# Performance work log

Hardware: AMD Instinct MI355X
Metric: run time of the kernel (lower is better)

## Reference

```python
import jax, jax.numpy as jnp
import numpy as np

B, S, N = 1, 128, 256
C_IN, C_H, C_OUT = 256, 32, 128
EPS = 1e-5


def setup_inputs() -> dict:
    key = jax.random.key(0)
    k_m, k_wa, k_wb, k_wo = jax.random.split(key, 4)
    m = jax.random.normal(k_m, (B, S, N, C_IN), dtype=jnp.float32)
    mask = jnp.ones((B, S, N), dtype=jnp.float32)
    gamma = jnp.ones((C_IN,), dtype=jnp.float32)
    beta = jnp.zeros((C_IN,), dtype=jnp.float32)
    # nn.Linear weights are (out, in)
    Wa = jax.random.normal(k_wa, (C_H, C_IN), dtype=jnp.float32) / np.sqrt(C_IN).astype(np.float32)
    Wb = jax.random.normal(k_wb, (C_H, C_IN), dtype=jnp.float32) / np.sqrt(C_IN).astype(np.float32)
    # proj_o is final_init (zeros) in the source; use small random weights so the
    # baseline output is non-trivial for correctness checking.
    Wo = jax.random.normal(k_wo, (C_OUT, C_H * C_H), dtype=jnp.float32) / np.sqrt(C_H * C_H).astype(np.float32)
    bo = jnp.zeros((C_OUT,), dtype=jnp.float32)
    return {"m": m, "mask": mask, "gamma": gamma, "beta": beta,
            "Wa": Wa, "Wb": Wb, "Wo": Wo, "bo": bo}


def reference(m, mask, gamma, beta, Wa, Wb, Wo, bo):
    # LayerNorm over c_in
    mu = jnp.mean(m, axis=-1, keepdims=True)
    var = jnp.mean((m - mu) ** 2, axis=-1, keepdims=True)
    mn = (m - mu) * jax.lax.rsqrt(var + EPS) * gamma + beta  # (B,S,N,c_in)

    mk = mask[..., None]  # (B,S,N,1)
    a = jnp.einsum('bsni,hi->bsnh', mn, Wa) * mk  # (B,S,N,c_h)
    b = jnp.einsum('bsni,hi->bsnh', mn, Wb) * mk  # (B,S,N,c_h)

    # pairwise mask count over S, clamped to >= 1
    num_mask = jnp.clip(jnp.einsum('bsi,bsj->bij', mask, mask), 1.0, None)  # (B,N,N)

    # outer-product mean over the sequence dim
    z = jnp.einsum('bsic,bsjd->bijcd', a, b)  # (B,N,N,c_h,c_h)
    z = z.reshape(z.shape[0], z.shape[1], z.shape[2], C_H * C_H)
    z = z / num_mask[..., None]

    return jnp.einsum('bijk,ok->bijo', z, Wo) + bo  # (B,N,N,c_out)
```

## Files before the change

### kernel.cpp

```cpp
#include <hip/hip_runtime.h>
#include <hip/hip_bf16.h>

#define S_DIM 128
#define N_DIM 256
#define CIN   256
#define CH    32
#define COUT  128

typedef __attribute__((ext_vector_type(8))) short bf16x8;
typedef __attribute__((ext_vector_type(4))) float f32x4;
typedef __attribute__((ext_vector_type(16))) float f32x16;

__device__ __forceinline__ unsigned short f2bf(float f) {
  union { float f; unsigned int u; } v; v.f = f;
  unsigned int u = v.u;
  return (unsigned short)((u + 0x7FFFu + ((u >> 16) & 1u)) >> 16);
}

__device__ __forceinline__ unsigned int pk2(float x, float y) {
  float2 f2; f2.x = x; f2.y = y;
  __hip_bfloat162 h = __float22bfloat162_rn(f2);
  union { __hip_bfloat162 h; unsigned int u; } c; c.h = h;
  return c.u;
}

__global__ __launch_bounds__(256) void lnp_prep_kernel(
    const float* __restrict__ m, const float* __restrict__ mask,
    const float* __restrict__ gamma, const float* __restrict__ beta,
    const float* __restrict__ Wa, const float* __restrict__ Wb,
    const float* __restrict__ Wo,
    float* __restrict__ rnm, unsigned short* __restrict__ wo3,
    unsigned short* __restrict__ a_t, unsigned short* __restrict__ b_t) {
  const int b = blockIdx.x, t = threadIdx.x;
  if (b < 1024) {
    __shared__ __align__(16) unsigned short mn[32][264];
    __shared__ __align__(16) unsigned short wabs[64 * 256];
    const int i = b & 255, s0 = (b >> 8) * 32;
    const int w = t >> 6, l = t & 63, lq = l >> 4, lr = l & 15;

    #pragma unroll
    for (int it = 0; it < 8; it++) {
      const int gi = it * 256 + t;
      const int r = gi >> 5, g = gi & 31;
      const float* src = (r < 32) ? (Wa + r * 256 + g * 8)
                                  : (Wb + (r - 32) * 256 + g * 8);
      const int gp = (g & 16) | ((g ^ (r & 15)) & 15);
      unsigned short* dst = &wabs[r * 256 + gp * 8];
      const float4 v0 = *(const float4*)(src);
      const float4 v1 = *(const float4*)(src + 4);
      dst[0] = f2bf(v0.x); dst[1] = f2bf(v0.y); dst[2] = f2bf(v0.z); dst[3] = f2bf(v0.w);
      dst[4] = f2bf(v1.x); dst[5] = f2bf(v1.y); dst[6] = f2bf(v1.z); dst[7] = f2bf(v1.w);
    }

    const float4 g4 = *(const float4*)(gamma + l * 4);
    const float4 b4 = *(const float4*)(beta + l * 4);

    for (int rr = 0; rr < 8; rr++) {
      const int r = w * 8 + rr;
      const int s = s0 + r;
      const float4 v = *(const float4*)(m + ((size_t)(s * N_DIM + i)) * CIN + l * 4);
      float sum = v.x + v.y + v.z + v.w;
      float sq  = v.x * v.x + v.y * v.y + v.z * v.z + v.w * v.w;
      #pragma unroll
      for (int off = 32; off > 0; off >>= 1) {
        sum += __shfl_down(sum, off);
        sq  += __shfl_down(sq, off);
      }
      sum = __shfl(sum, 0); sq = __shfl(sq, 0);
      const float mu = sum * (1.0f / CIN);
      const float var = fmaxf(sq * (1.0f / CIN) - mu * mu, 0.0f);
      const float rs = rsqrtf(var + 1e-5f);
      const float mk = mask[s * N_DIM + i];
      ushort4 p;
      p.x = f2bf(((v.x - mu) * rs * g4.x + b4.x) * mk);
      p.y = f2bf(((v.y - mu) * rs * g4.y + b4.y) * mk);
      p.z = f2bf(((v.z - mu) * rs * g4.z + b4.z) * mk);
      p.w = f2bf(((v.w - mu) * rs * g4.w + b4.w) * mk);
      *(ushort4*)(&mn[r][l * 4]) = p;
    }
    __syncthreads();

    const int wm = w & 1;
    const int n2 = w >> 1;
    f32x4 acc0 = {0.f, 0.f, 0.f, 0.f}, acc1 = {0.f, 0.f, 0.f, 0.f};
    #pragma unroll
    for (int ks = 0; ks < 8; ks++) {
      const int k0 = ks * 32 + lq * 8;
      const int g = ks * 4 + lq;
      const int gp = (g & 16) | ((g ^ lr) & 15);
      const bf16x8 af = *(const bf16x8*)(&mn[wm * 16 + lr][k0]);
      const bf16x8 bf0 = *(const bf16x8*)(&wabs[(n2 * 32 + lr) * 256 + gp * 8]);
      const bf16x8 bf1 = *(const bf16x8*)(&wabs[(n2 * 32 + 16 + lr) * 256 + gp * 8]);
      acc0 = __builtin_amdgcn_mfma_f32_16x16x32_bf16(af, bf0, acc0, 0, 0, 0);
      acc1 = __builtin_amdgcn_mfma_f32_16x16x32_bf16(af, bf1, acc1, 0, 0, 0);
    }

    unsigned short* dst = (n2 == 0) ? a_t : b_t;
    const int scol = s0 + wm * 16 + lq * 4;
    ushort4 q0, q1;
    q0.x = f2bf(acc0[0]); q0.y = f2bf(acc0[1]); q0.z = f2bf(acc0[2]); q0.w = f2bf(acc0[3]);
    q1.x = f2bf(acc1[0]); q1.y = f2bf(acc1[1]); q1.z = f2bf(acc1[2]); q1.w = f2bf(acc1[3]);
    *(ushort4*)(dst + ((size_t)(i * CH + lr)) * S_DIM + scol) = q0;
    *(ushort4*)(dst + ((size_t)(i * CH + 16 + lr)) * S_DIM + scol) = q1;
  } else if (b < 1152) {
    const int r = b - 1024;
    #pragma unroll
    for (int q = 0; q < 4; q++) {
      const int f = r * 1024 + q * 256 + t;
      const int e = f & 7, l = (f >> 3) & 63;
      const int step = (f >> 9) & 63, og = f >> 15;
      const int kp = step * 16 + (l >> 5) * 8 + e;
      const int c = kp & 31, d = kp >> 5;
      const int o = og * 32 + (l & 31);
      wo3[f] = f2bf(Wo[o * 1024 + c * 32 + d]);
    }
  } else {
    const int i = b - 1152;
    float acc = 0.f;
    #pragma unroll 8
    for (int s = 0; s < S_DIM; s++)
      acc += mask[s * N_DIM + i] * mask[s * N_DIM + t];
    acc = fmaxf(acc, 1.0f);
    rnm[i * N_DIM + t] = 1.0f / acc;
  }
}

__global__ __launch_bounds__(1024, 4) void fused_kernel(
    const unsigned short* __restrict__ a_t, const unsigned short* __restrict__ b_t,
    const unsigned short* __restrict__ wo3, const float* __restrict__ rnm,
    const float* __restrict__ bo, float* __restrict__ out) {
  extern __shared__ __align__(16) unsigned short smem[];
  unsigned short* sA = smem;
  unsigned short* sB = smem + 32768;
  unsigned short* sZ = smem;
  float* fpart = (float*)smem;

  const int t = threadIdx.x, w = t >> 6, l = t & 63;
  const int lq = l >> 4, lr = l & 15;
  const int bx = blockIdx.x, by = blockIdx.y;

  const unsigned short* srcA = a_t + (size_t)bx * 32768;
  const unsigned short* srcB = b_t + (size_t)by * 32768;
  #pragma unroll
  for (int it = 0; it < 4; it++) {
    const int idx = it * 1024 + t;
    const int r = idx >> 4, g = idx & 15;
    const int dst = r * 128 + ((g ^ (r & 15)) * 8);
    *(bf16x8*)(&sA[dst]) = *(const bf16x8*)(srcA + idx * 8);
    *(bf16x8*)(&sB[dst]) = *(const bf16x8*)(srcB + idx * 8);
  }
  __syncthreads();

  const int wy = (w >> 2) * 64, wx = (w & 3) * 64;
  f32x4 acc[4][4];
  #pragma unroll
  for (int a = 0; a < 4; a++)
    #pragma unroll
    for (int c = 0; c < 4; c++) acc[a][c] = (f32x4){0.f, 0.f, 0.f, 0.f};

  #pragma unroll
  for (int ks = 0; ks < 4; ks++) {
    const int g0 = ks * 4 + lq;
    bf16x8 afr[4], bfr[4];
    #pragma unroll
    for (int a = 0; a < 4; a++) {
      const int ra = wy + a * 16 + lr;
      afr[a] = *(const bf16x8*)(&sA[ra * 128 + ((g0 ^ (ra & 15)) * 8)]);
      const int rb = wx + a * 16 + lr;
      bfr[a] = *(const bf16x8*)(&sB[rb * 128 + ((g0 ^ (rb & 15)) * 8)]);
    }
    #pragma unroll
    for (int a = 0; a < 4; a++)
      #pragma unroll
      for (int c = 0; c < 4; c++)
        acc[a][c] = __builtin_amdgcn_mfma_f32_16x16x32_bf16(afr[a], bfr[c], acc[a][c], 0, 0, 0);
  }
  __syncthreads();

  #pragma unroll
  for (int a = 0; a < 4; a++) {
    #pragma unroll
    for (int c = 0; c < 4; c++) {
      const int zrb = wy + a * 16 + lq * 4;
      const int zc  = wx + c * 16 + lr;
      const int pr = (zrb >> 5) * 8 + (zc >> 5);
      const int off = (zc & 31) * 32 + (zrb & 31);
      const int g = off >> 3;
      const int gp = (g & ~7) | ((g ^ (g >> 3) ^ pr) & 7);
      uint2 q;
      q.x = pk2(acc[a][c][0], acc[a][c][1]);
      q.y = pk2(acc[a][c][2], acc[a][c][3]);
      *(uint2*)(&sZ[pr * 1024 + gp * 8 + (off & 7)]) = q;
    }
  }
  __syncthreads();

  const int og = w & 3, kq = w >> 2;
  const int pA = l & 31, pB = 32 + pA;
  const unsigned short* wop =
      wo3 + ((size_t)(og * 64 + kq * 16) * 64 + l) * 8;
  f32x16 accA, accB;
  #pragma unroll
  for (int r = 0; r < 16; r++) { accA[r] = 0.f; accB[r] = 0.f; }

  #pragma unroll 8
  for (int j = 0; j < 16; j++) {
    const int s = kq * 16 + j;
    const int g = s * 2 + (l >> 5);
    const int gA = (g & ~7) | ((g ^ (g >> 3) ^ pA) & 7);
    const int gB = (g & ~7) | ((g ^ (g >> 3) ^ pB) & 7);
    const bf16x8 zfA = *(const bf16x8*)(&sZ[pA * 1024 + gA * 8]);
    const bf16x8 zfB = *(const bf16x8*)(&sZ[pB * 1024 + gB * 8]);
    const bf16x8 wf = *(const bf16x8*)(wop + (size_t)j * 512);
    accA = __builtin_amdgcn_mfma_f32_32x32x16_bf16(zfA, wf, accA, 0, 0, 0);
    accB = __builtin_amdgcn_mfma_f32_32x32x16_bf16(zfB, wf, accB, 0, 0, 0);
  }
  __syncthreads();

  const int oc = og * 32 + (l & 31);
  #pragma unroll
  for (int r = 0; r < 16; r++) {
    const int row = (r & 3) + 8 * (r >> 2) + 4 * (l >> 5);
    const int xo = oc ^ ((r & 3) << 3);
    fpart[kq * 8192 + row * 128 + xo] = accA[r];
    fpart[kq * 8192 + (row + 32) * 128 + xo] = accB[r];
  }
  __syncthreads();

  const int pair = t >> 4;
  const int ob   = (t & 15) * 8;
  const float4 bo0 = *(const float4*)(bo + ob);
  const float4 bo1 = *(const float4*)(bo + ob + 4);
  const int opc = pair * 128 + (ob ^ ((pair & 3) << 3));

  const int ii = bx * 8 + (pair >> 3), jj = by * 8 + (pair & 7);
  const float sc = rnm[ii * N_DIM + jj];

  f32x4 u0 = {0.f, 0.f, 0.f, 0.f}, u1 = {0.f, 0.f, 0.f, 0.f};
  #pragma unroll
  for (int q = 0; q < 4; q++) {
    u0 += *(const f32x4*)(&fpart[q * 8192 + opc]);
    u1 += *(const f32x4*)(&fpart[q * 8192 + opc + 4]);
  }
  float* po = out + ((size_t)(ii * N_DIM + jj)) * COUT + ob;
  float4 w0, w1;
  w0.x = u0[0] * sc + bo0.x; w0.y = u0[1] * sc + bo0.y;
  w0.z = u0[2] * sc + bo0.z; w0.w = u0[3] * sc + bo0.w;
  w1.x = u1[0] * sc + bo1.x; w1.y = u1[1] * sc + bo1.y;
  w1.z = u1[2] * sc + bo1.z; w1.w = u1[3] * sc + bo1.w;
  *(float4*)(po)     = w0;
  *(float4*)(po + 4) = w1;
}

extern "C" void kernel_launch(void* const* d_in, const int* in_sizes, int n_in,
                              void* d_out, int out_size, void* d_ws, size_t ws_size,
                              hipStream_t stream) {
  const float* m     = (const float*)d_in[0];
  const float* mask  = (const float*)d_in[1];
  const float* gamma = (const float*)d_in[2];
  const float* beta  = (const float*)d_in[3];
  const float* Wa    = (const float*)d_in[4];
  const float* Wb    = (const float*)d_in[5];
  const float* Wo    = (const float*)d_in[6];
  const float* bo    = (const float*)d_in[7];
  float* out = (float*)d_out;

  char* ws = (char*)d_ws;
  float*          rnm = (float*)(ws);
  unsigned short* wo3 = (unsigned short*)(ws + 262144);
  unsigned short* a_t = (unsigned short*)(ws + 524288);
  unsigned short* b_t = (unsigned short*)(ws + 2621440);

  hipFuncSetAttribute((const void*)fused_kernel,
                      hipFuncAttributeMaxDynamicSharedMemorySize, 131072);

  lnp_prep_kernel<<<1408, 256, 0, stream>>>(m, mask, gamma, beta, Wa, Wb, Wo,
                                            rnm, wo3, a_t, b_t);
  fused_kernel<<<dim3(32, 32), 1024, 131072, stream>>>(a_t, b_t, wo3, rnm, bo, out);
}
```

Before: 151.7 us.

## Halve fused block tile to 8x4 pairs with K-split staging to cut LDS

Each block of the fused kernel now covers 8 i by 4 j pairs with 512 threads instead of 8x8 with 1024, doubling the grid to 32x64. The A/B operands are staged through LDS in two K-halves, so dynamic shared memory drops from 128 KB to 64 KB. This should allow more blocks per CU and better latency hiding. In exchange it adds a sync between the halves and doubles total global reads of the a_t/wo3 operands. The split-K reduction layout is also simplified to padded rows.

```diff
diff --git a/kernel.cpp b/kernel.cpp
--- a/kernel.cpp
+++ b/kernel.cpp
@@ -125,13 +125,13 @@
   }
 }
 
-__global__ __launch_bounds__(1024, 4) void fused_kernel(
+__global__ __launch_bounds__(512, 4) void fused_kernel(
     const unsigned short* __restrict__ a_t, const unsigned short* __restrict__ b_t,
     const unsigned short* __restrict__ wo3, const float* __restrict__ rnm,
     const float* __restrict__ bo, float* __restrict__ out) {
   extern __shared__ __align__(16) unsigned short smem[];
   unsigned short* sA = smem;
-  unsigned short* sB = smem + 32768;
+  unsigned short* sB = smem + 16384;
   unsigned short* sZ = smem;
   float* fpart = (float*)smem;
 
@@ -140,40 +140,51 @@
   const int bx = blockIdx.x, by = blockIdx.y;
 
   const unsigned short* srcA = a_t + (size_t)bx * 32768;
-  const unsigned short* srcB = b_t + (size_t)by * 32768;
-  #pragma unroll
-  for (int it = 0; it < 4; it++) {
-    const int idx = it * 1024 + t;
-    const int r = idx >> 4, g = idx & 15;
-    const int dst = r * 128 + ((g ^ (r & 15)) * 8);
-    *(bf16x8*)(&sA[dst]) = *(const bf16x8*)(srcA + idx * 8);
-    *(bf16x8*)(&sB[dst]) = *(const bf16x8*)(srcB + idx * 8);
-  }
-  __syncthreads();
-
-  const int wy = (w >> 2) * 64, wx = (w & 3) * 64;
+  const unsigned short* srcB = b_t + (size_t)by * 16384;
+
+  const int wy = (w >> 1) * 64, wx = (w & 1) * 64;
   f32x4 acc[4][4];
   #pragma unroll
   for (int a = 0; a < 4; a++)
     #pragma unroll
     for (int c = 0; c < 4; c++) acc[a][c] = (f32x4){0.f, 0.f, 0.f, 0.f};
 
-  #pragma unroll
-  for (int ks = 0; ks < 4; ks++) {
-    const int g0 = ks * 4 + lq;
-    bf16x8 afr[4], bfr[4];
-    #pragma unroll
-    for (int a = 0; a < 4; a++) {
-      const int ra = wy + a * 16 + lr;
-      afr[a] = *(const bf16x8*)(&sA[ra * 128 + ((g0 ^ (ra & 15)) * 8)]);
-      const int rb = wx + a * 16 + lr;
-      bfr[a] = *(const bf16x8*)(&sB[rb * 128 + ((g0 ^ (rb & 15)) * 8)]);
-    }
-    #pragma unroll
-    for (int a = 0; a < 4; a++)
+  #pragma unroll 1
+  for (int h = 0; h < 2; h++) {
+    if (h) __syncthreads();
+    #pragma unroll
+    for (int it = 0; it < 4; it++) {
+      const int idx = it * 512 + t;
+      const int r = idx >> 3, g = idx & 7;
+      const bf16x8 v = *(const bf16x8*)(srcA + r * 128 + h * 64 + g * 8);
+      *(bf16x8*)(&sA[r * 64 + ((g ^ (r & 7)) << 3)]) = v;
+    }
+    #pragma unroll
+    for (int it = 0; it < 2; it++) {
+      const int idx = it * 512 + t;
+      const int r = idx >> 3, g = idx & 7;
+      const bf16x8 v = *(const bf16x8*)(srcB + r * 128 + h * 64 + g * 8);
+      *(bf16x8*)(&sB[r * 64 + ((g ^ (r & 7)) << 3)]) = v;
+    }
+    __syncthreads();
+
+    #pragma unroll
+    for (int ks2 = 0; ks2 < 2; ks2++) {
+      const int gi = ks2 * 4 + lq;
+      bf16x8 afr[4], bfr[4];
       #pragma unroll
-      for (int c = 0; c < 4; c++)
-        acc[a][c] = __builtin_amdgcn_mfma_f32_16x16x32_bf16(afr[a], bfr[c], acc[a][c], 0, 0, 0);
+      for (int a = 0; a < 4; a++) {
+        const int ra = wy + a * 16 + lr;
+        afr[a] = *(const bf16x8*)(&sA[ra * 64 + ((gi ^ (ra & 7)) << 3)]);
+        const int rb = wx + a * 16 + lr;
+        bfr[a] = *(const bf16x8*)(&sB[rb * 64 + ((gi ^ (rb & 7)) << 3)]);
+      }
+      #pragma unroll
+      for (int a = 0; a < 4; a++)
+        #pragma unroll
+        for (int c = 0; c < 4; c++)
+          acc[a][c] = __builtin_amdgcn_mfma_f32_16x16x32_bf16(afr[a], bfr[c], acc[a][c], 0, 0, 0);
+    }
   }
   __syncthreads();
 
@@ -183,7 +194,7 @@
     for (int c = 0; c < 4; c++) {
       const int zrb = wy + a * 16 + lq * 4;
       const int zc  = wx + c * 16 + lr;
-      const int pr = (zrb >> 5) * 8 + (zc >> 5);
+      const int pr = (zrb >> 5) * 4 + (zc >> 5);
       const int off = (zc & 31) * 32 + (zrb & 31);
       const int g = off >> 3;
       const int gp = (g & ~7) | ((g ^ (g >> 3) ^ pr) & 7);
@@ -195,25 +206,22 @@
   }
   __syncthreads();
 
-  const int og = w & 3, kq = w >> 2;
-  const int pA = l & 31, pB = 32 + pA;
+  const int og = w & 3, kh = w >> 2;
+  const int pA = l & 31;
   const unsigned short* wop =
-      wo3 + ((size_t)(og * 64 + kq * 16) * 64 + l) * 8;
-  f32x16 accA, accB;
-  #pragma unroll
-  for (int r = 0; r < 16; r++) { accA[r] = 0.f; accB[r] = 0.f; }
+      wo3 + ((size_t)(og * 64 + kh * 32) * 64 + l) * 8;
+  f32x16 acc2;
+  #pragma unroll
+  for (int r = 0; r < 16; r++) acc2[r] = 0.f;
 
   #pragma unroll 8
-  for (int j = 0; j < 16; j++) {
-    const int s = kq * 16 + j;
+  for (int j = 0; j < 32; j++) {
+    const int s = kh * 32 + j;
     const int g = s * 2 + (l >> 5);
     const int gA = (g & ~7) | ((g ^ (g >> 3) ^ pA) & 7);
-    const int gB = (g & ~7) | ((g ^ (g >> 3) ^ pB) & 7);
-    const bf16x8 zfA = *(const bf16x8*)(&sZ[pA * 1024 + gA * 8]);
-    const bf16x8 zfB = *(const bf16x8*)(&sZ[pB * 1024 + gB * 8]);
+    const bf16x8 zf = *(const bf16x8*)(&sZ[pA * 1024 + gA * 8]);
     const bf16x8 wf = *(const bf16x8*)(wop + (size_t)j * 512);
-    accA = __builtin_amdgcn_mfma_f32_32x32x16_bf16(zfA, wf, accA, 0, 0, 0);
-    accB = __builtin_amdgcn_mfma_f32_32x32x16_bf16(zfB, wf, accB, 0, 0, 0);
+    acc2 = __builtin_amdgcn_mfma_f32_32x32x16_bf16(zf, wf, acc2, 0, 0, 0);
   }
   __syncthreads();
 
@@ -221,9 +229,7 @@
   #pragma unroll
   for (int r = 0; r < 16; r++) {
     const int row = (r & 3) + 8 * (r >> 2) + 4 * (l >> 5);
-    const int xo = oc ^ ((r & 3) << 3);
-    fpart[kq * 8192 + row * 128 + xo] = accA[r];
-    fpart[kq * 8192 + (row + 32) * 128 + xo] = accB[r];
+    fpart[kh * 4224 + row * 132 + oc] = acc2[r];
   }
   __syncthreads();
 
@@ -231,16 +237,16 @@
   const int ob   = (t & 15) * 8;
   const float4 bo0 = *(const float4*)(bo + ob);
   const float4 bo1 = *(const float4*)(bo + ob + 4);
-  const int opc = pair * 128 + (ob ^ ((pair & 3) << 3));
-
-  const int ii = bx * 8 + (pair >> 3), jj = by * 8 + (pair & 7);
+
+  const int ii = bx * 8 + (pair >> 2), jj = by * 4 + (pair & 3);
   const float sc = rnm[ii * N_DIM + jj];
 
+  const int fb = pair * 132 + ob;
   f32x4 u0 = {0.f, 0.f, 0.f, 0.f}, u1 = {0.f, 0.f, 0.f, 0.f};
   #pragma unroll
-  for (int q = 0; q < 4; q++) {
-    u0 += *(const f32x4*)(&fpart[q * 8192 + opc]);
-    u1 += *(const f32x4*)(&fpart[q * 8192 + opc + 4]);
+  for (int q = 0; q < 2; q++) {
+    u0 += *(const f32x4*)(&fpart[q * 4224 + fb]);
+    u1 += *(const f32x4*)(&fpart[q * 4224 + fb + 4]);
   }
   float* po = out + ((size_t)(ii * N_DIM + jj)) * COUT + ob;
   float4 w0, w1;
@@ -272,9 +278,9 @@
   unsigned short* b_t = (unsigned short*)(ws + 2621440);
 
   hipFuncSetAttribute((const void*)fused_kernel,
-                      hipFuncAttributeMaxDynamicSharedMemorySize, 131072);
+                      hipFuncAttributeMaxDynamicSharedMemorySize, 65536);
 
   lnp_prep_kernel<<<1408, 256, 0, stream>>>(m, mask, gamma, beta, Wa, Wb, Wo,
                                             rnm, wo3, a_t, b_t);
-  fused_kernel<<<dim3(32, 32), 1024, 131072, stream>>>(a_t, b_t, wo3, rnm, bo, out);
-}
+  fused_kernel<<<dim3(32, 64), 512, 65536, stream>>>(a_t, b_t, wo3, rnm, bo, out);
+}
```

New measurement: 147.0 us. 3.1% less time.
